# Performance work log

Hardware: AMD Instinct MI355X
Metric: run time of the kernel (lower is better)

## Reference

```python
import jax, jax.numpy as jnp
import numpy as np

SR = 44100        # sample rate (init kwarg)
WINDOWS = 2048    # fft window size (init kwarg)
B, P = 128, 192   # batch, number of peaking filters


def setup_inputs() -> dict:
    key = jax.random.key(0)
    k1, k2, k3 = jax.random.split(key, 3)
    # center frequencies in (40 Hz, 0.45*sr), gains in dB, quality factors in [0.5, 2)
    center = jax.random.uniform(k1, (B, P), minval=40.0, maxval=0.45 * SR, dtype=jnp.float32)
    gain = 6.0 * jax.random.normal(k2, (B, P), dtype=jnp.float32)
    q = jax.random.uniform(k3, (B, P), minval=0.5, maxval=2.0, dtype=jnp.float32)
    return {"center": center, "gain": gain, "q": q}


def _biquad(a, b, windows):
    # a, b: [..., 3] filter taps; rfft zero-pads to `windows` samples.
    iir = jnp.fft.rfft(a, n=windows, axis=-1)  # [..., windows//2+1] complex
    fir = jnp.fft.rfft(b, n=windows, axis=-1)
    return fir / iir


def reference(center, gain, q):
    """Peaking equalizer: [..., windows//2+1] complex frequency response."""
    w0 = (2.0 * np.pi / SR) * center
    A = jnp.exp(gain * (np.log(10.0) / 40.0))
    alpha = jnp.sin(w0) / 2.0 / q
    cos_w0 = jnp.cos(w0)
    b0 = 1.0 + alpha * A
    b1 = -2.0 * cos_w0
    b2 = 1.0 - alpha * A
    a0 = 1.0 + alpha / A
    a1 = -2.0 * cos_w0
    a2 = 1.0 - alpha / A
    return _biquad(jnp.stack([a0, a1, a2], axis=-1),
                   jnp.stack([b0, b1, b2], axis=-1), WINDOWS)
```

## Files before the change

kernel.cpp:

```cpp
#include <hip/hip_runtime.h>
#include <math.h>

constexpr int NBINS = 1025;
constexpr int NROWS = 128 * 192;

__device__ inline unsigned int f2bf(float f) {
    unsigned int u = __float_as_uint(f);
    return (u + 0x7FFFu + ((u >> 16) & 1u)) >> 16;
}

__global__ __launch_bounds__(256) void eq_kernel(
    const float* __restrict__ center,
    const float* __restrict__ gain,
    const float* __restrict__ q,
    unsigned int* __restrict__ out)
{
    __shared__ float p[4];
    const int row = blockIdx.x;
    if (threadIdx.x == 0) {
        float w0 = 1.4247585730565955e-4f * center[row];
        float sh, ch;
        sincosf(0.5f * w0, &sh, &ch);
        float A = exp2f(0.08304820237218406f * gain[row]);
        float alpha = sh * ch / q[row];
        float g2 = alpha / A;
        p[0] = sh;
        p[1] = alpha * alpha;
        p[2] = g2;
        p[3] = alpha * A - g2;
    }
    __syncthreads();
    const float sh = p[0], a2 = p[1], g2 = p[2], gd = p[3];

    unsigned int* __restrict__ orow = out + (size_t)row * NBINS;
    for (int k = threadIdx.x; k < NBINS; k += 256) {
        float h = (float)k * 1.5339807878856412e-3f;
        float st, ct;
        sincosf(h, &st, &ct);
        float d  = 2.0f * (sh - st) * (sh + st);
        float s  = 2.0f * st * ct;
        float d2 = d * d;
        float g2s = g2 * s;
        float den = fmaf(g2s, g2s, d2);
        float inv = __builtin_amdgcn_rcpf(den);
        float re = fmaf(a2, s * s, d2) * inv;
        float im = gd * s * d * inv;
        orow[k] = f2bf(im) | (f2bf(re) << 16);
    }
}

extern "C" void kernel_launch(void* const* d_in, const int* in_sizes, int n_in,
                              void* d_out, int out_size, void* d_ws, size_t ws_size,
                              hipStream_t stream) {
    const float* center = (const float*)d_in[0];
    const float* gain   = (const float*)d_in[1];
    const float* q      = (const float*)d_in[2];
    eq_kernel<<<NROWS, 256, 0, stream>>>(center, gain, q, (unsigned int*)d_out);
}
```

Baseline: 135.8 us.

## Process 16 rows per block with shared sin/cos table and 16-byte stores

Each block now handles 16 filter rows. A per-block shared-memory table of sin/cos over the 1025 bins replaces per-element sincosf calls, and per-row parameters are computed by 16 threads in parallel. Output is written as uint4 over the block's contiguous span, so stores are 16 bytes wide and no longer misaligned at row boundaries. This costs an integer divide per element to recover the row and bin, plus shared-memory reads, and the grid shrinks to 1536 blocks.

```diff
diff --git a/kernel.cpp b/kernel.cpp
--- a/kernel.cpp
+++ b/kernel.cpp
@@ -3,6 +3,10 @@
 
 constexpr int NBINS = 1025;
 constexpr int NROWS = 128 * 192;
+constexpr int RPB   = 16;
+constexpr int NBLK  = NROWS / RPB;
+constexpr int DWB   = RPB * NBINS;
+constexpr int QPB   = DWB / 4;
 
 __device__ inline unsigned int f2bf(float f) {
     unsigned int u = __float_as_uint(f);
@@ -15,37 +19,49 @@
     const float* __restrict__ q,
     unsigned int* __restrict__ out)
 {
-    __shared__ float p[4];
-    const int row = blockIdx.x;
-    if (threadIdx.x == 0) {
+    __shared__ float2 tab[NBINS];
+    __shared__ float4 rp[RPB];
+
+    const int tid = threadIdx.x;
+    if (tid < RPB) {
+        const int row = blockIdx.x * RPB + tid;
         float w0 = 1.4247585730565955e-4f * center[row];
         float sh, ch;
         sincosf(0.5f * w0, &sh, &ch);
         float A = exp2f(0.08304820237218406f * gain[row]);
         float alpha = sh * ch / q[row];
         float g2 = alpha / A;
-        p[0] = sh;
-        p[1] = alpha * alpha;
-        p[2] = g2;
-        p[3] = alpha * A - g2;
+        rp[tid] = make_float4(sh, alpha * alpha, g2, alpha * A - g2);
+    }
+    for (int k = tid; k < NBINS; k += 256) {
+        float st, ct;
+        sincosf((float)k * 1.5339807878856412e-3f, &st, &ct);
+        tab[k] = make_float2(st, ct);
     }
     __syncthreads();
-    const float sh = p[0], a2 = p[1], g2 = p[2], gd = p[3];
 
-    unsigned int* __restrict__ orow = out + (size_t)row * NBINS;
-    for (int k = threadIdx.x; k < NBINS; k += 256) {
-        float h = (float)k * 1.5339807878856412e-3f;
-        float st, ct;
-        sincosf(h, &st, &ct);
-        float d  = 2.0f * (sh - st) * (sh + st);
-        float s  = 2.0f * st * ct;
-        float d2 = d * d;
-        float g2s = g2 * s;
-        float den = fmaf(g2s, g2s, d2);
-        float inv = __builtin_amdgcn_rcpf(den);
-        float re = fmaf(a2, s * s, d2) * inv;
-        float im = gd * s * d * inv;
-        orow[k] = f2bf(im) | (f2bf(re) << 16);
+    uint4* __restrict__ ob = (uint4*)(out + (size_t)blockIdx.x * DWB);
+    for (int g = tid; g < QPB; g += 256) {
+        const int f0 = 4 * g;
+        unsigned int w[4];
+        #pragma unroll
+        for (int j = 0; j < 4; ++j) {
+            const int f = f0 + j;
+            const int r = f / NBINS;
+            const int k = f - r * NBINS;
+            const float4 P = rp[r];
+            const float2 t = tab[k];
+            float d  = 2.0f * (P.x - t.x) * (P.x + t.x);
+            float s  = 2.0f * t.x * t.y;
+            float d2 = d * d;
+            float g2s = P.z * s;
+            float den = fmaf(g2s, g2s, d2);
+            float inv = __builtin_amdgcn_rcpf(den);
+            float re = fmaf(P.y, s * s, d2) * inv;
+            float im = P.w * s * d * inv;
+            w[j] = f2bf(im) | (f2bf(re) << 16);
+        }
+        ob[g] = make_uint4(w[0], w[1], w[2], w[3]);
     }
 }
 
@@ -55,5 +71,5 @@
     const float* center = (const float*)d_in[0];
     const float* gain   = (const float*)d_in[1];
     const float* q      = (const float*)d_in[2];
-    eq_kernel<<<NROWS, 256, 0, stream>>>(center, gain, q, (unsigned int*)d_out);
+    eq_kernel<<<NBLK, 256, 0, stream>>>(center, gain, q, (unsigned int*)d_out);
 }
```

After: 115.3 us. 15.1% less time.
